# Kernel tuning notes

Hardware: AMD Instinct MI355X
Metric: run time of the kernel (lower is better)

Reference implementation:

```python
import jax, jax.numpy as jnp
import numpy as np
import math

NUM_CLASSES = 80
FPN_CH = 256
STEM = [256, 256, 256, 256]
C_IN = {"c3": 64, "c4": 160, "c5": 400}


def _conv(x, w, b, pad):
    # x: (B, Cin, H, W), w: (Cout, Cin, kh, kw)
    y = jax.lax.conv_general_dilated(
        x, w, window_strides=(1, 1), padding=[(pad, pad), (pad, pad)],
        dimension_numbers=("NCHW", "OIHW", "NCHW"))
    return y + b[None, :, None, None]


def _upsample2x(x):
    # F.interpolate(scale_factor=2), default mode='nearest'
    return jnp.repeat(jnp.repeat(x, 2, axis=2), 2, axis=3)


def _flatten_hw(x):
    # (B, C, H, W) -> (B, H*W, C)
    B, C, H, W = x.shape
    return x.reshape(B, C, H * W).transpose(0, 2, 1)


def setup_inputs() -> dict:
    key = jax.random.key(0)
    ks = iter(jax.random.split(key, 64))
    d = {}
    d["c3"] = jax.random.normal(next(ks), (2, 64, 64, 64), jnp.float32)
    d["c4"] = jax.random.normal(next(ks), (2, 160, 32, 32), jnp.float32)
    d["c5"] = jax.random.normal(next(ks), (2, 400, 16, 16), jnp.float32)

    def w(shape, std):
        return jax.random.normal(next(ks), shape, jnp.float32) * std

    # FPN lateral 1x1 convs and output 3x3 convs (default torch init ~ small)
    for lvl, cin in C_IN.items():
        n = lvl[1]
        d[f"lat{n}_w"] = w((FPN_CH, cin, 1, 1), 1.0 / math.sqrt(cin))
        d[f"lat{n}_b"] = jnp.zeros((FPN_CH,), jnp.float32)
        d[f"out{n}_w"] = w((FPN_CH, FPN_CH, 3, 3), 1.0 / math.sqrt(9 * FPN_CH))
        d[f"out{n}_b"] = jnp.zeros((FPN_CH,), jnp.float32)

    # Stem convs: init N(0, 0.01), bias 0 (per module code). Stacked (L, Cout, Cin, 3, 3).
    L = len(STEM)
    d["stem_cls_w"] = w((L, FPN_CH, FPN_CH, 3, 3), 0.01)
    d["stem_cls_b"] = jnp.zeros((L, FPN_CH), jnp.float32)
    d["stem_box_w"] = w((L, FPN_CH, FPN_CH, 3, 3), 0.01)
    d["stem_box_b"] = jnp.zeros((L, FPN_CH), jnp.float32)

    d["cls_w"] = w((NUM_CLASSES, FPN_CH, 3, 3), 1.0 / math.sqrt(9 * FPN_CH))
    d["cls_b"] = jnp.full((NUM_CLASSES,), -math.log(99.0), jnp.float32)
    d["box_w"] = w((4, FPN_CH, 3, 3), 1.0 / math.sqrt(9 * FPN_CH))
    d["box_b"] = jnp.zeros((4,), jnp.float32)
    d["ctr_w"] = w((1, FPN_CH, 3, 3), 1.0 / math.sqrt(9 * FPN_CH))
    d["ctr_b"] = jnp.zeros((1,), jnp.float32)
    return d


def reference(c3, c4, c5,
              lat3_w, lat3_b, lat4_w, lat4_b, lat5_w, lat5_b,
              out3_w, out3_b, out4_w, out4_b, out5_w, out5_b,
              stem_cls_w, stem_cls_b, stem_box_w, stem_box_b,
              cls_w, cls_b, box_w, box_b, ctr_w, ctr_b):
    # ---- FPN ----
    l3 = _conv(c3, lat3_w, lat3_b, 0)
    l4 = _conv(c4, lat4_w, lat4_b, 0)
    l5 = _conv(c5, lat5_w, lat5_b, 0)
    p5 = _conv(l5, out5_w, out5_b, 1)
    l4 = l4 + _upsample2x(l5)
    p4 = _conv(l4, out4_w, out4_b, 1)
    l3 = l3 + _upsample2x(l4)
    p3 = _conv(l3, out3_w, out3_b, 1)

    # ---- Prediction heads ----
    def head(feat):
        hc, hb = feat, feat
        for i in range(stem_cls_w.shape[0]):
            hc = jax.nn.relu(_conv(hc, stem_cls_w[i], stem_cls_b[i], 1))
            hb = jax.nn.relu(_conv(hb, stem_box_w[i], stem_box_b[i], 1))
        cls = _flatten_hw(_conv(hc, cls_w, cls_b, 1))      # (B, HW, num_classes)
        box = _flatten_hw(_conv(hb, box_w, box_b, 1))      # (B, HW, 4)
        ctr = _flatten_hw(_conv(hb, ctr_w, ctr_b, 1))      # (B, HW, 1)
        return cls, box, ctr

    outs = [head(p) for p in (p3, p4, p5)]
    cls_all = jnp.concatenate([o[0] for o in outs], axis=1)
    box_all = jnp.concatenate([o[1] for o in outs], axis=1)
    ctr_all = jnp.concatenate([o[2] for o in outs], axis=1)
    # pack: (B, total_locations, num_classes + 4 + 1)
    return jnp.concatenate([cls_all, box_all, ctr_all], axis=-1)
```

## Files before the change

kernel.cpp:

```cpp
#include <hip/hip_runtime.h>

typedef unsigned short u16;
typedef __attribute__((ext_vector_type(8))) __bf16 bf16x8;
typedef __attribute__((ext_vector_type(16))) float f32x16;

__device__ __forceinline__ float bf2f(u16 u) {
  union { unsigned i; float f; } x; x.i = ((unsigned)u) << 16; return x.f;
}
__device__ __forceinline__ u16 f2bf(float f) {
  union { float f; unsigned i; } x; x.f = f;
  unsigned r = x.i + 0x7FFFu + ((x.i >> 16) & 1u);
  return (u16)(r >> 16);
}
__device__ __forceinline__ bf16x8 ld8(const u16* p) {
  union { int2 i2[2]; bf16x8 v; } u;
  u.i2[0] = *(const int2*)p;
  u.i2[1] = *(const int2*)(p + 4);
  return u.v;
}

struct WJob { const float* src; u16* dst; int Cin, Cout, taps, NC, Cpad, special; };
struct WArgs {
  WJob j[16];
  const float *box_w, *ctr_w;
  const float *cls_b, *box_b, *ctr_b;
  float *bcls, *bbc;
};

__global__ __launch_bounds__(256) void wtrans_kernel(WArgs a) {
  WJob jb = a.j[blockIdx.y];
  int count = jb.taps * jb.NC * jb.Cpad * 64;
  for (int e = blockIdx.x * 256 + threadIdx.x; e < count; e += gridDim.x * 256) {
    int cw = e & 63;
    int r = e >> 6;
    int n = r % jb.Cpad;
    int q = r / jb.Cpad;
    int t = q % jb.taps;
    int cc = q / jb.taps;
    int ci = cc * 64 + cw;
    int nl = (n & ~63) + 2 * (n & 31) + ((n >> 5) & 1);
    float v = 0.f;
    if (jb.special) {
      if (ci < jb.Cin) {
        if (nl < 4) v = a.box_w[((size_t)nl * jb.Cin + ci) * jb.taps + t];
        else if (nl == 4) v = a.ctr_w[(size_t)ci * jb.taps + t];
      }
    } else if (nl < jb.Cout && ci < jb.Cin) {
      v = jb.src[((size_t)nl * jb.Cin + ci) * jb.taps + t];
    }
    jb.dst[e] = f2bf(v);
  }
  if (blockIdx.y == 0 && blockIdx.x == 0) {
    int t = threadIdx.x;
    if (t < 128) a.bcls[t] = (t < 80) ? a.cls_b[t] : 0.f;
    else if (t < 192) {
      int n = t - 128;
      a.bbc[n] = (n < 4) ? a.box_b[n] : (n == 4 ? a.ctr_b[0] : 0.f);
    }
  }
}

__global__ __launch_bounds__(256) void transpose_kernel(const float* __restrict__ c3,
                                                        const float* __restrict__ c4,
                                                        const float* __restrict__ c5,
                                                        u16* __restrict__ c3t,
                                                        u16* __restrict__ c4t,
                                                        u16* __restrict__ c5t) {
  int gid = blockIdx.x * 256 + threadIdx.x;
  const float* in; u16* out; int C, HW;
  if (gid < 524288) { in = c3; out = c3t; C = 64; HW = 4096; }
  else if (gid < 851968) { gid -= 524288; in = c4; out = c4t; C = 160; HW = 1024; }
  else { gid -= 851968; if (gid >= 204800) return; in = c5; out = c5t; C = 400; HW = 256; }
  int CHW = C * HW;
  int b = gid / CHW;
  int rem = gid - b * CHW;
  int c = rem / HW;
  int pos = rem - c * HW;
  out[((size_t)b * HW + pos) * C + c] = f2bf(in[gid]);
}

__global__ __launch_bounds__(256) void upadd2_kernel(u16* __restrict__ l3, u16* __restrict__ l4n,
                                                     const u16* __restrict__ l4,
                                                     const u16* __restrict__ l5) {
  int gid = blockIdx.x * 256 + threadIdx.x;
  if (gid < 524288) {
    int c = gid & 255; int m = gid >> 8;
    int b = m >> 10, pos = m & 1023;
    int y = pos >> 5, x = pos & 31;
    int sp = (b << 8) + ((y >> 1) << 4) + (x >> 1);
    l4n[gid] = f2bf(bf2f(l4[gid]) + bf2f(l5[(size_t)sp * 256 + c]));
  } else {
    int g2 = gid - 524288;
    int c = g2 & 255; int m = g2 >> 8;
    int b = m >> 12, pos = m & 4095;
    int y = pos >> 6, x = pos & 63;
    int sp2 = (b << 10) + ((y >> 1) << 5) + (x >> 1);
    int sp4 = (b << 8) + ((y >> 2) << 4) + (x >> 2);
    l3[g2] = f2bf(bf2f(l3[g2]) + bf2f(l4[(size_t)sp2 * 256 + c]) + bf2f(l5[(size_t)sp4 * 256 + c]));
  }
}

struct ConvP {
  const u16* src[2][3];
  const u16* wT[2][3];
  const float* bias[2][3];
  void* dst[2][3];
  int H[3], W[3], lgW[3], lgHW[3], pre[3], NC[3], Crow[3], locoff[3];
  int Cpad[2], Nvalid[2], choff[2], ny[2];
  int relu, direct;
};

#define APAD 68

#define TAPX(RB) do {                                                          \
    if (kk + 1 < ktot) {                                                       \
      writeB((kk + 1) & 1, RB);                                                \
      if (kk + 3 < ktot) loadB(kk + 3, RB);                                    \
    }                                                                          \
    int hpo = 0;                                                               \
    if (TAPS == 9) { int q_ = (t * 11) >> 5; hpo = t + 7 * q_ - 11; }          \
    const int hp = hpbase + hpo;                                               \
    const u16* ar = As + hp * APAD + koffs;                                    \
    const u16* br0 = Bs[kk & 1] + (lane & 31) * APAD + koffs;                  \
    const u16* br1 = br0 + 32 * APAD;                                          \
    _Pragma("unroll")                                                          \
    for (int ks = 0; ks < 4; ++ks) {                                           \
      bf16x8 af = ld8(ar + ks * 16);                                           \
      acc[0] = __builtin_amdgcn_mfma_f32_32x32x16_bf16(af, ld8(br0 + ks * 16), acc[0], 0, 0, 0); \
      acc[1] = __builtin_amdgcn_mfma_f32_32x32x16_bf16(af, ld8(br1 + ks * 16), acc[1], 0, 0, 0); \
    }                                                                          \
    __syncthreads();                                                           \
    ++t; ++kk;                                                                 \
    if (t == TAPS) {                                                           \
      t = 0; ++cc;                                                             \
      if (cc < NCv) {                                                          \
        writeA(rA);                                                           \
        if (cc + 1 < NCv) loadA(cc + 1, rA);                                   \
        __syncthreads();                                                       \
      }                                                                        \
    }                                                                          \
  } while (0)

template <int TAPS>
__global__ __launch_bounds__(256, 3) void conv_kernel(ConvP p) {
  constexpr int HALO_W = (TAPS == 9) ? 10 : 8;
  constexpr int HROWS = (TAPS == 9) ? 18 : 16;
  constexpr int NA = HROWS * HALO_W * 8;
  constexpr int NSLOT = (NA + 255) / 256;
  constexpr int OFF = (TAPS == 9) ? 1 : 0;
  __shared__ u16 As[180 * APAD];
  __shared__ u16 Bs[2][64 * APAD];
  const int tid = threadIdx.x;
  const int br = blockIdx.z;
  if (blockIdx.y >= p.ny[br]) return;
  const int bx = blockIdx.x;
  const int lv = (bx >= p.pre[1]) + (bx >= p.pre[2]);
  const u16* __restrict__ src = p.src[br][lv];
  const u16* __restrict__ wT = p.wT[br][lv];
  const float* bias = p.bias[br][lv];
  void* dstv = p.dst[br][lv];
  const int H = p.H[lv], W = p.W[lv];
  const int lgWv = p.lgW[lv], lgHWv = p.lgHW[lv];
  const int NCv = p.NC[lv], Crow = p.Crow[lv];
  const int Cpadv = p.Cpad[br];
  const int ktot = NCv * TAPS;
  const int nt = blockIdx.y * 64;
  const int wave = tid >> 6, lane = tid & 63;

  const int pidx = bx - p.pre[lv];
  const int lgppb = lgHWv - 7;
  const int lgnpx = lgWv - 3;
  const int batch = pidx >> lgppb;
  const int pp = pidx & ((1 << lgppb) - 1);
  const int py0 = (pp >> lgnpx) << 4;
  const int px0 = (pp & ((1 << lgnpx) - 1)) << 3;
  const size_t srcb = (size_t)batch * (1 << lgHWv) * Crow;

  f32x16 acc[2];
#pragma unroll
  for (int i = 0; i < 16; ++i) { acc[0][i] = 0.f; acc[1][i] = 0.f; }

  const int ml = wave * 32 + (lane & 31);
  const int my = ml >> 3, mx = ml & 7;
  const int koffs = (lane >> 5) << 3;
  const int hpbase = (my + OFF) * HALO_W + (mx + OFF);

  int4 rA[NSLOT];
  int4 rB0[2], rB1[2];

  auto loadA = [&](int cc2, int4* r) {
    int kb = cc2 << 6;
#pragma unroll
    for (int s = 0; s < NSLOT; ++s) {
      int idx = s * 256 + tid;
      int4 v = make_int4(0, 0, 0, 0);
      if (idx < NA) {
        int pos = idx >> 3, part = idx & 7;
        int hy = pos / HALO_W, hx = pos - hy * HALO_W;
        int gy = py0 + hy - OFF, gx = px0 + hx - OFF;
        int ch = kb + (part << 3);
        if ((unsigned)gy < (unsigned)H && (unsigned)gx < (unsigned)W && ch < Crow)
          v = *(const int4*)(src + srcb + (size_t)((gy << lgWv) + gx) * Crow + ch);
      }
      r[s] = v;
    }
  };
  auto writeA = [&](const int4* r) {
#pragma unroll
    for (int s = 0; s < NSLOT; ++s) {
      int idx = s * 256 + tid;
      if (idx < NA) {
        int pos = idx >> 3, part = idx & 7;
        u16* d = As + pos * APAD + (part << 3);
        *(int2*)d = make_int2(r[s].x, r[s].y);
        *(int2*)(d + 4) = make_int2(r[s].z, r[s].w);
      }
    }
  };
  auto loadB = [&](int j, int4* r) {
    const u16* wsrc = wT + (((size_t)j * Cpadv + nt) << 6);
    r[0] = *(const int4*)(wsrc + ((tid >> 3) << 6) + ((tid & 7) << 3));
    r[1] = *(const int4*)(wsrc + (((tid >> 3) + 32) << 6) + ((tid & 7) << 3));
  };
  auto writeB = [&](int bufi, const int4* r) {
    u16* bb = Bs[bufi];
    u16* d0 = bb + (tid >> 3) * APAD + ((tid & 7) << 3);
    u16* d1 = bb + ((tid >> 3) + 32) * APAD + ((tid & 7) << 3);
    *(int2*)d0 = make_int2(r[0].x, r[0].y);
    *(int2*)(d0 + 4) = make_int2(r[0].z, r[0].w);
    *(int2*)d1 = make_int2(r[1].x, r[1].y);
    *(int2*)(d1 + 4) = make_int2(r[1].z, r[1].w);
  };

  loadA(0, rA);
  loadB(0, rB0);
  if (ktot > 1) loadB(1, rB1);
  writeA(rA);
  writeB(0, rB0);
  if (ktot > 2) loadB(2, rB0);
  if (NCv > 1) loadA(1, rA);
  __syncthreads();

  int kk = 0, t = 0, cc = 0;
  while (true) {
    TAPX(rB1);
    if (kk >= ktot) break;
    TAPX(rB0);
    if (kk >= ktot) break;
  }

  const int col = lane & 31;
  const int rbs = 4 * (lane >> 5);
  const float bv0 = bias[nt + 2 * col];
  const float bv1 = bias[nt + 2 * col + 1];
#pragma unroll
  for (int r = 0; r < 16; ++r) {
    int m2 = wave * 32 + rbs + (r & 3) + 8 * (r >> 2);
    int posi = ((py0 + (m2 >> 3)) << lgWv) + px0 + (m2 & 7);
    float v0 = acc[0][r] + bv0;
    float v1 = acc[1][r] + bv1;
    if (p.relu) { v0 = fmaxf(v0, 0.f); v1 = fmaxf(v1, 0.f); }
    if (!p.direct) {
      unsigned pk = (unsigned)f2bf(v0) | ((unsigned)f2bf(v1) << 16);
      *(unsigned*)((u16*)dstv + ((size_t)(batch << lgHWv) + posi) * 256 + nt + 2 * col) = pk;
    } else {
      int n0 = nt + 2 * col;
      float* dd = (float*)dstv + ((size_t)(batch * 5376 + p.locoff[lv] + posi)) * 85 + p.choff[br];
      if (n0 < p.Nvalid[br]) dd[n0] = v0;
      if (n0 + 1 < p.Nvalid[br]) dd[n0 + 1] = v1;
    }
  }
}

extern "C" void kernel_launch(void* const* d_in, const int* in_sizes, int n_in,
                              void* d_out, int out_size, void* d_ws, size_t ws_size,
                              hipStream_t stream) {
  (void)in_sizes; (void)n_in; (void)out_size; (void)ws_size;
  const float* c3 = (const float*)d_in[0];
  const float* c4 = (const float*)d_in[1];
  const float* c5 = (const float*)d_in[2];
  const float* lat_w[3] = {(const float*)d_in[3], (const float*)d_in[7], (const float*)d_in[11]};
  const float* lat_b[3] = {(const float*)d_in[4], (const float*)d_in[8], (const float*)d_in[12]};
  const float* out_w[3] = {(const float*)d_in[5], (const float*)d_in[9], (const float*)d_in[13]};
  const float* out_b[3] = {(const float*)d_in[6], (const float*)d_in[10], (const float*)d_in[14]};
  const float* scw = (const float*)d_in[15];
  const float* scb = (const float*)d_in[16];
  const float* sbw = (const float*)d_in[17];
  const float* sbb = (const float*)d_in[18];
  const float* clsw = (const float*)d_in[19];
  const float* clsb = (const float*)d_in[20];
  const float* boxw = (const float*)d_in[21];
  const float* boxb = (const float*)d_in[22];
  const float* ctrw = (const float*)d_in[23];
  const float* ctrb = (const float*)d_in[24];
  float* out = (float*)d_out;
  u16* ws = (u16*)d_ws;

  size_t o = 0;
  auto alloc = [&](size_t n) { size_t r = o; o += (n + 127) & ~(size_t)127; return ws + r; };

  u16* c3t = alloc(524288);
  u16* c4t = alloc(327680);
  u16* c5t = alloc(204800);
  u16* l3 = alloc(2097152);
  u16* l4 = alloc(524288);
  u16* l4n = alloc(524288);
  u16* l5 = alloc(131072);
  u16* p3 = alloc(2097152);
  u16* p4 = alloc(524288);
  u16* p5 = alloc(131072);
  const size_t hsz[3] = {2097152, 524288, 131072};
  u16 *hc[2][3], *hb[2][3];
  for (int ab = 0; ab < 2; ++ab)
    for (int lvv = 0; lvv < 3; ++lvv) { hc[ab][lvv] = alloc(hsz[lvv]); hb[ab][lvv] = alloc(hsz[lvv]); }
  const int latCin[3] = {64, 160, 400};
  const int latNC[3] = {1, 3, 7};
  u16* wl[3]; for (int i = 0; i < 3; ++i) wl[i] = alloc((size_t)latNC[i] * 256 * 64);
  u16* wo[3]; for (int i = 0; i < 3; ++i) wo[i] = alloc(589824);
  u16* wsc[4]; for (int i = 0; i < 4; ++i) wsc[i] = alloc(589824);
  u16* wsb[4]; for (int i = 0; i < 4; ++i) wsb[i] = alloc(589824);
  u16* wcls = alloc(294912);
  u16* wbc = alloc(147456);
  float* bcls = (float*)alloc(256);
  float* bbc = (float*)alloc(128);

  WArgs wa;
  int ji = 0;
  for (int i = 0; i < 3; ++i) wa.j[ji++] = WJob{lat_w[i], wl[i], latCin[i], 256, 1, latNC[i], 256, 0};
  for (int i = 0; i < 3; ++i) wa.j[ji++] = WJob{out_w[i], wo[i], 256, 256, 9, 4, 256, 0};
  for (int i = 0; i < 4; ++i) wa.j[ji++] = WJob{scw + (size_t)i * 589824, wsc[i], 256, 256, 9, 4, 256, 0};
  for (int i = 0; i < 4; ++i) wa.j[ji++] = WJob{sbw + (size_t)i * 589824, wsb[i], 256, 256, 9, 4, 256, 0};
  wa.j[ji++] = WJob{clsw, wcls, 256, 80, 9, 4, 128, 0};
  wa.j[ji++] = WJob{nullptr, wbc, 256, 5, 9, 4, 64, 1};
  wa.box_w = boxw; wa.ctr_w = ctrw;
  wa.cls_b = clsb; wa.box_b = boxb; wa.ctr_b = ctrb; wa.bcls = bcls; wa.bbc = bbc;
  wtrans_kernel<<<dim3(96, 16), dim3(256), 0, stream>>>(wa);

  transpose_kernel<<<dim3(4128), dim3(256), 0, stream>>>(c3, c4, c5, c3t, c4t, c5t);

  const int Hs[3] = {64, 32, 16};
  const int lgWs[3] = {6, 5, 4}, lgHWs[3] = {12, 10, 8};

  auto setLv = [&](ConvP& p, int i, int lvv) {
    p.H[i] = Hs[lvv]; p.W[i] = Hs[lvv]; p.lgW[i] = lgWs[lvv]; p.lgHW[i] = lgHWs[lvv];
  };

  {
    ConvP p{};
    const u16* srcs[3] = {c3t, c4t, c5t};
    u16* dsts[3] = {l3, l4, l5};
    for (int i = 0; i < 3; ++i) {
      p.src[0][i] = srcs[i]; p.wT[0][i] = wl[i]; p.bias[0][i] = lat_b[i]; p.dst[0][i] = dsts[i];
      setLv(p, i, i);
      p.NC[i] = latNC[i]; p.Crow[i] = latCin[i]; p.locoff[i] = 0;
    }
    p.pre[0] = 0; p.pre[1] = 64; p.pre[2] = 80;
    p.Cpad[0] = 256; p.Nvalid[0] = 0; p.choff[0] = 0; p.ny[0] = 4;
    p.relu = 0; p.direct = 0;
    conv_kernel<1><<<dim3(84, 4, 1), dim3(256), 0, stream>>>(p);
  }

  upadd2_kernel<<<dim3(10240), dim3(256), 0, stream>>>(l3, l4n, l4, l5);

  {
    ConvP p{};
    const u16* srcs[3] = {l3, l4n, l5};
    u16* dsts[3] = {p3, p4, p5};
    for (int i = 0; i < 3; ++i) {
      p.src[0][i] = srcs[i]; p.wT[0][i] = wo[i]; p.bias[0][i] = out_b[i]; p.dst[0][i] = dsts[i];
      setLv(p, i, i);
      p.NC[i] = 4; p.Crow[i] = 256; p.locoff[i] = 0;
    }
    p.pre[0] = 0; p.pre[1] = 64; p.pre[2] = 80;
    p.Cpad[0] = 256; p.Nvalid[0] = 0; p.choff[0] = 0; p.ny[0] = 4;
    p.relu = 0; p.direct = 0;
    conv_kernel<9><<<dim3(84, 4, 1), dim3(256), 0, stream>>>(p);
  }

  u16* pin[3] = {p3, p4, p5};
  for (int i = 0; i < 4; ++i) {
    ConvP p{};
    int di = i & 1;
    for (int lvv = 0; lvv < 3; ++lvv) {
      const u16 *s0, *s1;
      if (i == 0) { s0 = pin[lvv]; s1 = pin[lvv]; }
      else { int si = (i - 1) & 1; s0 = hc[si][lvv]; s1 = hb[si][lvv]; }
      p.src[0][lvv] = s0; p.src[1][lvv] = s1;
      p.wT[0][lvv] = wsc[i]; p.wT[1][lvv] = wsb[i];
      p.bias[0][lvv] = scb + i * 256; p.bias[1][lvv] = sbb + i * 256;
      p.dst[0][lvv] = hc[di][lvv]; p.dst[1][lvv] = hb[di][lvv];
      setLv(p, lvv, lvv);
      p.NC[lvv] = 4; p.Crow[lvv] = 256; p.locoff[lvv] = 0;
    }
    p.pre[0] = 0; p.pre[1] = 64; p.pre[2] = 80;
    p.Cpad[0] = 256; p.Cpad[1] = 256;
    p.Nvalid[0] = 0; p.Nvalid[1] = 0; p.choff[0] = 0; p.choff[1] = 0;
    p.ny[0] = 4; p.ny[1] = 4;
    p.relu = 1; p.direct = 0;
    conv_kernel<9><<<dim3(84, 4, 2), dim3(256), 0, stream>>>(p);
  }

  {
    const int locoffs[3] = {0, 4096, 5120};
    ConvP p{};
    for (int lvv = 0; lvv < 3; ++lvv) {
      p.src[0][lvv] = hc[1][lvv]; p.wT[0][lvv] = wcls; p.bias[0][lvv] = bcls; p.dst[0][lvv] = out;
      p.src[1][lvv] = hb[1][lvv]; p.wT[1][lvv] = wbc; p.bias[1][lvv] = bbc; p.dst[1][lvv] = out;
      setLv(p, lvv, lvv);
      p.NC[lvv] = 4; p.Crow[lvv] = 256; p.locoff[lvv] = locoffs[lvv];
    }
    p.pre[0] = 0; p.pre[1] = 64; p.pre[2] = 80;
    p.Cpad[0] = 128; p.Cpad[1] = 64;
    p.Nvalid[0] = 80; p.Nvalid[1] = 5;
    p.choff[0] = 0; p.choff[1] = 80;
    p.ny[0] = 2; p.ny[1] = 1;
    p.relu = 0; p.direct = 1;
    conv_kernel<9><<<dim3(84, 2, 2), dim3(256), 0, stream>>>(p);
  }
}
```

Before: 366.9 us.

## Split conv kernel into specialized 1x1 and fully unrolled 3x3 variants with 3-tap weight staging

```diff
diff --git a/kernel.cpp b/kernel.cpp
--- a/kernel.cpp
+++ b/kernel.cpp
@@ -117,10 +117,7 @@
       writeB((kk + 1) & 1, RB);                                                \
       if (kk + 3 < ktot) loadB(kk + 3, RB);                                    \
     }                                                                          \
-    int hpo = 0;                                                               \
-    if (TAPS == 9) { int q_ = (t * 11) >> 5; hpo = t + 7 * q_ - 11; }          \
-    const int hp = hpbase + hpo;                                               \
-    const u16* ar = As + hp * APAD + koffs;                                    \
+    const u16* ar = As + hpbase * APAD + koffs;                                \
     const u16* br0 = Bs[kk & 1] + (lane & 31) * APAD + koffs;                  \
     const u16* br1 = br0 + 32 * APAD;                                          \
     _Pragma("unroll")                                                          \
@@ -130,25 +127,19 @@
       acc[1] = __builtin_amdgcn_mfma_f32_32x32x16_bf16(af, ld8(br1 + ks * 16), acc[1], 0, 0, 0); \
     }                                                                          \
     __syncthreads();                                                           \
-    ++t; ++kk;                                                                 \
-    if (t == TAPS) {                                                           \
-      t = 0; ++cc;                                                             \
-      if (cc < NCv) {                                                          \
-        writeA(rA);                                                           \
-        if (cc + 1 < NCv) loadA(cc + 1, rA);                                   \
-        __syncthreads();                                                       \
-      }                                                                        \
+    ++kk; ++cc;                                                                \
+    if (cc < NCv) {                                                            \
+      writeA(rA);                                                              \
+      if (cc + 1 < NCv) loadA(cc + 1, rA);                                     \
+      __syncthreads();                                                         \
     }                                                                          \
   } while (0)
 
-template <int TAPS>
-__global__ __launch_bounds__(256, 3) void conv_kernel(ConvP p) {
-  constexpr int HALO_W = (TAPS == 9) ? 10 : 8;
-  constexpr int HROWS = (TAPS == 9) ? 18 : 16;
-  constexpr int NA = HROWS * HALO_W * 8;
-  constexpr int NSLOT = (NA + 255) / 256;
-  constexpr int OFF = (TAPS == 9) ? 1 : 0;
-  __shared__ u16 As[180 * APAD];
+__global__ __launch_bounds__(256, 3) void conv1_kernel(ConvP p) {
+  constexpr int HALO_W = 8;
+  constexpr int NA = 16 * 8 * 8;
+  constexpr int NSLOT = 4;
+  __shared__ u16 As[128 * APAD];
   __shared__ u16 Bs[2][64 * APAD];
   const int tid = threadIdx.x;
   const int br = blockIdx.z;
@@ -163,7 +154,7 @@
   const int lgWv = p.lgW[lv], lgHWv = p.lgHW[lv];
   const int NCv = p.NC[lv], Crow = p.Crow[lv];
   const int Cpadv = p.Cpad[br];
-  const int ktot = NCv * TAPS;
+  const int ktot = NCv;
   const int nt = blockIdx.y * 64;
   const int wave = tid >> 6, lane = tid & 63;
 
@@ -183,10 +174,138 @@
   const int ml = wave * 32 + (lane & 31);
   const int my = ml >> 3, mx = ml & 7;
   const int koffs = (lane >> 5) << 3;
-  const int hpbase = (my + OFF) * HALO_W + (mx + OFF);
+  const int hpbase = my * HALO_W + mx;
 
   int4 rA[NSLOT];
   int4 rB0[2], rB1[2];
+
+  auto loadA = [&](int cc2, int4* r) {
+    int kb = cc2 << 6;
+#pragma unroll
+    for (int s = 0; s < NSLOT; ++s) {
+      int idx = s * 256 + tid;
+      int4 v = make_int4(0, 0, 0, 0);
+      int pos = idx >> 3, part = idx & 7;
+      int hy = pos >> 3, hx = pos & 7;
+      int gy = py0 + hy, gx = px0 + hx;
+      int ch = kb + (part << 3);
+      if ((unsigned)gy < (unsigned)H && (unsigned)gx < (unsigned)W && ch < Crow)
+        v = *(const int4*)(src + srcb + (size_t)((gy << lgWv) + gx) * Crow + ch);
+      r[s] = v;
+    }
+  };
+  auto writeA = [&](const int4* r) {
+#pragma unroll
+    for (int s = 0; s < NSLOT; ++s) {
+      int idx = s * 256 + tid;
+      int pos = idx >> 3, part = idx & 7;
+      u16* d = As + pos * APAD + (part << 3);
+      *(int2*)d = make_int2(r[s].x, r[s].y);
+      *(int2*)(d + 4) = make_int2(r[s].z, r[s].w);
+    }
+  };
+  auto loadB = [&](int j, int4* r) {
+    const u16* wsrc = wT + (((size_t)j * Cpadv + nt) << 6);
+    r[0] = *(const int4*)(wsrc + ((tid >> 3) << 6) + ((tid & 7) << 3));
+    r[1] = *(const int4*)(wsrc + (((tid >> 3) + 32) << 6) + ((tid & 7) << 3));
+  };
+  auto writeB = [&](int bufi, const int4* r) {
+    u16* bb = Bs[bufi];
+    u16* d0 = bb + (tid >> 3) * APAD + ((tid & 7) << 3);
+    u16* d1 = bb + ((tid >> 3) + 32) * APAD + ((tid & 7) << 3);
+    *(int2*)d0 = make_int2(r[0].x, r[0].y);
+    *(int2*)(d0 + 4) = make_int2(r[0].z, r[0].w);
+    *(int2*)d1 = make_int2(r[1].x, r[1].y);
+    *(int2*)(d1 + 4) = make_int2(r[1].z, r[1].w);
+  };
+
+  loadA(0, rA);
+  loadB(0, rB0);
+  if (ktot > 1) loadB(1, rB1);
+  writeA(rA);
+  writeB(0, rB0);
+  if (ktot > 2) loadB(2, rB0);
+  if (NCv > 1) loadA(1, rA);
+  __syncthreads();
+
+  int kk = 0, cc = 0;
+  while (true) {
+    TAPX(rB1);
+    if (kk >= ktot) break;
+    TAPX(rB0);
+    if (kk >= ktot) break;
+  }
+
+  const int col = lane & 31;
+  const int rbs = 4 * (lane >> 5);
+  const float bv0 = bias[nt + 2 * col];
+  const float bv1 = bias[nt + 2 * col + 1];
+#pragma unroll
+  for (int r = 0; r < 16; ++r) {
+    int m2 = wave * 32 + rbs + (r & 3) + 8 * (r >> 2);
+    int posi = ((py0 + (m2 >> 3)) << lgWv) + px0 + (m2 & 7);
+    float v0 = acc[0][r] + bv0;
+    float v1 = acc[1][r] + bv1;
+    unsigned pk = (unsigned)f2bf(v0) | ((unsigned)f2bf(v1) << 16);
+    *(unsigned*)((u16*)dstv + ((size_t)(batch << lgHWv) + posi) * 256 + nt + 2 * col) = pk;
+  }
+}
+
+#define TAP9(T, S) do {                                                        \
+    constexpr int hpo_ = ((T) / 3 - 1) * 10 + ((T) % 3 - 1);                   \
+    const u16* ar = As + (hpbase + hpo_) * APAD + koffs;                       \
+    const u16* br0 = Bs[S] + (lane & 31) * APAD + koffs;                       \
+    const u16* br1 = br0 + 32 * APAD;                                          \
+    _Pragma("unroll")                                                          \
+    for (int ks = 0; ks < 4; ++ks) {                                           \
+      bf16x8 af = ld8(ar + ks * 16);                                           \
+      acc[0] = __builtin_amdgcn_mfma_f32_32x32x16_bf16(af, ld8(br0 + ks * 16), acc[0], 0, 0, 0); \
+      acc[1] = __builtin_amdgcn_mfma_f32_32x32x16_bf16(af, ld8(br1 + ks * 16), acc[1], 0, 0, 0); \
+    }                                                                          \
+  } while (0)
+
+__global__ __launch_bounds__(256, 3) void conv9_kernel(ConvP p) {
+  constexpr int HALO_W = 10;
+  constexpr int NA = 18 * 10 * 8;
+  constexpr int NSLOT = 6;
+  __shared__ u16 As[180 * APAD];
+  __shared__ u16 Bs[3][64 * APAD];
+  const int tid = threadIdx.x;
+  const int br = blockIdx.z;
+  if (blockIdx.y >= p.ny[br]) return;
+  const int bx = blockIdx.x;
+  const int lv = (bx >= p.pre[1]) + (bx >= p.pre[2]);
+  const u16* __restrict__ src = p.src[br][lv];
+  const u16* __restrict__ wT = p.wT[br][lv];
+  const float* bias = p.bias[br][lv];
+  void* dstv = p.dst[br][lv];
+  const int H = p.H[lv], W = p.W[lv];
+  const int lgWv = p.lgW[lv], lgHWv = p.lgHW[lv];
+  const int Crow = p.Crow[lv];
+  const int Cpadv = p.Cpad[br];
+  const int nt = blockIdx.y * 64;
+  const int wave = tid >> 6, lane = tid & 63;
+
+  const int pidx = bx - p.pre[lv];
+  const int lgppb = lgHWv - 7;
+  const int lgnpx = lgWv - 3;
+  const int batch = pidx >> lgppb;
+  const int pp = pidx & ((1 << lgppb) - 1);
+  const int py0 = (pp >> lgnpx) << 4;
+  const int px0 = (pp & ((1 << lgnpx) - 1)) << 3;
+  const size_t srcb = (size_t)batch * (1 << lgHWv) * Crow;
+
+  f32x16 acc[2];
+#pragma unroll
+  for (int i = 0; i < 16; ++i) { acc[0][i] = 0.f; acc[1][i] = 0.f; }
+
+  const int ml = wave * 32 + (lane & 31);
+  const int my = ml >> 3, mx = ml & 7;
+  const int koffs = (lane >> 5) << 3;
+  const int hpbase = (my + 1) * HALO_W + (mx + 1);
+
+  int4 rA[NSLOT];
+  int4 rB[6];
 
   auto loadA = [&](int cc2, int4* r) {
     int kb = cc2 << 6;
@@ -197,7 +316,7 @@
       if (idx < NA) {
         int pos = idx >> 3, part = idx & 7;
         int hy = pos / HALO_W, hx = pos - hy * HALO_W;
-        int gy = py0 + hy - OFF, gx = px0 + hx - OFF;
+        int gy = py0 + hy - 1, gx = px0 + hx - 1;
         int ch = kb + (part << 3);
         if ((unsigned)gy < (unsigned)H && (unsigned)gx < (unsigned)W && ch < Crow)
           v = *(const int4*)(src + srcb + (size_t)((gy << lgWv) + gx) * Crow + ch);
@@ -217,42 +336,62 @@
       }
     }
   };
-  auto loadB = [&](int j, int4* r) {
-    const u16* wsrc = wT + (((size_t)j * Cpadv + nt) << 6);
-    r[0] = *(const int4*)(wsrc + ((tid >> 3) << 6) + ((tid & 7) << 3));
-    r[1] = *(const int4*)(wsrc + (((tid >> 3) + 32) << 6) + ((tid & 7) << 3));
-  };
-  auto writeB = [&](int bufi, const int4* r) {
-    u16* bb = Bs[bufi];
-    u16* d0 = bb + (tid >> 3) * APAD + ((tid & 7) << 3);
-    u16* d1 = bb + ((tid >> 3) + 32) * APAD + ((tid & 7) << 3);
-    *(int2*)d0 = make_int2(r[0].x, r[0].y);
-    *(int2*)(d0 + 4) = make_int2(r[0].z, r[0].w);
-    *(int2*)d1 = make_int2(r[1].x, r[1].y);
-    *(int2*)(d1 + 4) = make_int2(r[1].z, r[1].w);
+  auto loadB3 = [&](int j, int4* r) {
+#pragma unroll
+    for (int s = 0; s < 3; ++s) {
+      const u16* wsrc = wT + (((size_t)(j + s) * Cpadv + nt) << 6);
+      r[2 * s] = *(const int4*)(wsrc + ((tid >> 3) << 6) + ((tid & 7) << 3));
+      r[2 * s + 1] = *(const int4*)(wsrc + (((tid >> 3) + 32) << 6) + ((tid & 7) << 3));
+    }
+  };
+  auto writeB3 = [&](const int4* r) {
+#pragma unroll
+    for (int s = 0; s < 3; ++s) {
+      u16* bb = Bs[s];
+      u16* d0 = bb + (tid >> 3) * APAD + ((tid & 7) << 3);
+      u16* d1 = bb + ((tid >> 3) + 32) * APAD + ((tid & 7) << 3);
+      *(int2*)d0 = make_int2(r[2 * s].x, r[2 * s].y);
+      *(int2*)(d0 + 4) = make_int2(r[2 * s].z, r[2 * s].w);
+      *(int2*)d1 = make_int2(r[2 * s + 1].x, r[2 * s + 1].y);
+      *(int2*)(d1 + 4) = make_int2(r[2 * s + 1].z, r[2 * s + 1].w);
+    }
   };
 
   loadA(0, rA);
-  loadB(0, rB0);
-  if (ktot > 1) loadB(1, rB1);
+  loadB3(0, rB);
   writeA(rA);
-  writeB(0, rB0);
-  if (ktot > 2) loadB(2, rB0);
-  if (NCv > 1) loadA(1, rA);
+  writeB3(rB);
+  loadB3(3, rB);
+  loadA(1, rA);
   __syncthreads();
 
-  int kk = 0, t = 0, cc = 0;
-  while (true) {
-    TAPX(rB1);
-    if (kk >= ktot) break;
-    TAPX(rB0);
-    if (kk >= ktot) break;
+  for (int cc = 0; cc < 4; ++cc) {
+    TAP9(0, 0); TAP9(1, 1); TAP9(2, 2);
+    __syncthreads();
+    writeB3(rB);
+    __syncthreads();
+    loadB3(cc * 9 + 6, rB);
+    TAP9(3, 0); TAP9(4, 1); TAP9(5, 2);
+    __syncthreads();
+    writeB3(rB);
+    __syncthreads();
+    if (cc * 9 + 9 < 36) loadB3(cc * 9 + 9, rB);
+    TAP9(6, 0); TAP9(7, 1); TAP9(8, 2);
+    __syncthreads();
+    if (cc < 3) {
+      writeB3(rB);
+      writeA(rA);
+      __syncthreads();
+      loadB3(cc * 9 + 12, rB);
+      if (cc < 2) loadA(cc + 2, rA);
+    }
   }
 
   const int col = lane & 31;
   const int rbs = 4 * (lane >> 5);
-  const float bv0 = bias[nt + 2 * col];
-  const float bv1 = bias[nt + 2 * col + 1];
+  const int nbase = nt + 2 * col;
+  const float bv0 = bias[nbase];
+  const float bv1 = bias[nbase + 1];
 #pragma unroll
   for (int r = 0; r < 16; ++r) {
     int m2 = wave * 32 + rbs + (r & 3) + 8 * (r >> 2);
@@ -262,12 +401,11 @@
     if (p.relu) { v0 = fmaxf(v0, 0.f); v1 = fmaxf(v1, 0.f); }
     if (!p.direct) {
       unsigned pk = (unsigned)f2bf(v0) | ((unsigned)f2bf(v1) << 16);
-      *(unsigned*)((u16*)dstv + ((size_t)(batch << lgHWv) + posi) * 256 + nt + 2 * col) = pk;
+      *(unsigned*)((u16*)dstv + ((size_t)(batch << lgHWv) + posi) * 256 + nbase) = pk;
     } else {
-      int n0 = nt + 2 * col;
       float* dd = (float*)dstv + ((size_t)(batch * 5376 + p.locoff[lv] + posi)) * 85 + p.choff[br];
-      if (n0 < p.Nvalid[br]) dd[n0] = v0;
-      if (n0 + 1 < p.Nvalid[br]) dd[n0 + 1] = v1;
+      if (nbase < p.Nvalid[br]) dd[nbase] = v0;
+      if (nbase + 1 < p.Nvalid[br]) dd[nbase + 1] = v1;
     }
   }
 }
@@ -323,6 +461,7 @@
   u16* wbc = alloc(147456);
   float* bcls = (float*)alloc(256);
   float* bbc = (float*)alloc(128);
+  alloc(2048);
 
   WArgs wa;
   int ji = 0;
@@ -340,7 +479,6 @@
 
   const int Hs[3] = {64, 32, 16};
   const int lgWs[3] = {6, 5, 4}, lgHWs[3] = {12, 10, 8};
-
   auto setLv = [&](ConvP& p, int i, int lvv) {
     p.H[i] = Hs[lvv]; p.W[i] = Hs[lvv]; p.lgW[i] = lgWs[lvv]; p.lgHW[i] = lgHWs[lvv];
   };
@@ -357,7 +495,7 @@
     p.pre[0] = 0; p.pre[1] = 64; p.pre[2] = 80;
     p.Cpad[0] = 256; p.Nvalid[0] = 0; p.choff[0] = 0; p.ny[0] = 4;
     p.relu = 0; p.direct = 0;
-    conv_kernel<1><<<dim3(84, 4, 1), dim3(256), 0, stream>>>(p);
+    conv1_kernel<<<dim3(84, 4, 1), dim3(256), 0, stream>>>(p);
   }
 
   upadd2_kernel<<<dim3(10240), dim3(256), 0, stream>>>(l3, l4n, l4, l5);
@@ -374,7 +512,7 @@
     p.pre[0] = 0; p.pre[1] = 64; p.pre[2] = 80;
     p.Cpad[0] = 256; p.Nvalid[0] = 0; p.choff[0] = 0; p.ny[0] = 4;
     p.relu = 0; p.direct = 0;
-    conv_kernel<9><<<dim3(84, 4, 1), dim3(256), 0, stream>>>(p);
+    conv9_kernel<<<dim3(84, 4, 1), dim3(256), 0, stream>>>(p);
   }
 
   u16* pin[3] = {p3, p4, p5};
@@ -397,7 +535,7 @@
     p.Nvalid[0] = 0; p.Nvalid[1] = 0; p.choff[0] = 0; p.choff[1] = 0;
     p.ny[0] = 4; p.ny[1] = 4;
     p.relu = 1; p.direct = 0;
-    conv_kernel<9><<<dim3(84, 4, 2), dim3(256), 0, stream>>>(p);
+    conv9_kernel<<<dim3(84, 4, 2), dim3(256), 0, stream>>>(p);
   }
 
   {
@@ -415,6 +553,6 @@
     p.choff[0] = 0; p.choff[1] = 80;
     p.ny[0] = 2; p.ny[1] = 1;
     p.relu = 0; p.direct = 1;
-    conv_kernel<9><<<dim3(84, 2, 2), dim3(256), 0, stream>>>(p);
-  }
-}
+    conv9_kernel<<<dim3(84, 2, 2), dim3(256), 0, stream>>>(p);
+  }
+}
```

Measured after the change: 360.9 us. About the same (-1.6%).
